# Optimization experiments

Measured on AMD Instinct MI355X. Metric: run time of the kernel, lower is better.

## Reference

```python
import jax, jax.numpy as jnp
import numpy as np

# ---- constants mirroring ATSSPostProcessor defaults / metainfo ----
PRE_NMS_THRESH = 0.05
PRE_NMS_TOP_N = 1000
NMS_THRESH = 0.6
POST_TOP_N = 100
IMG_H, IMG_W = 800.0, 1216.0      # metainfo img_shape
BW_XY, BW_WH = 10.0, 5.0          # GLIP/ATSS box coder weights (10,10,5,5)
MAX_DWH = float(np.log(1000.0 / 16.0))
CLASS_OFFSET = 10000.0            # batched_nms class offset (> max coord)


def setup_inputs() -> dict:
    key = jax.random.key(0)
    k0, k1, k2, k3 = jax.random.split(key, 4)
    N, C, L, H, W = 8, 80, 256, 100, 152
    box_regression = jax.random.normal(k0, (N, 4, H, W), jnp.float32)
    centerness = jax.random.normal(k1, (N, 1, H, W), jnp.float32)
    box_cls = jax.random.normal(k2, (N, C, H, W), jnp.float32)
    dot_product_logits = jax.random.normal(k3, (N, H * W, L), jnp.float32)
    # stride-8 grid anchors with base size 64
    ys, xs = np.meshgrid(np.arange(H), np.arange(W), indexing='ij')
    cx, cy = (xs + 0.5) * 8.0, (ys + 0.5) * 8.0
    anchors = jnp.asarray(
        np.stack([cx - 32, cy - 32, cx + 32, cy + 32], -1).reshape(-1, 4),
        jnp.float32)
    # MEAN aggregation positive map: class j <- tokens [3j, 3j+1, 3j+2]
    pm = np.zeros((C, L), np.float32)
    for j in range(C):
        pm[j, 3 * j:3 * j + 3] = 1.0 / 3.0
    pos_map = jnp.asarray(pm)
    return dict(box_regression=box_regression, centerness=centerness,
                box_cls=box_cls, dot_product_logits=dot_product_logits,
                anchors=anchors, pos_map=pos_map)


def _decode(a, r):
    # delta_xywh decode with weights (10,10,5,5), clamped to img_shape
    aw, ah = a[..., 2] - a[..., 0], a[..., 3] - a[..., 1]
    acx, acy = a[..., 0] + 0.5 * aw, a[..., 1] + 0.5 * ah
    dx, dy = r[..., 0] / BW_XY, r[..., 1] / BW_XY
    dw = jnp.minimum(r[..., 2] / BW_WH, MAX_DWH)
    dh = jnp.minimum(r[..., 3] / BW_WH, MAX_DWH)
    pcx, pcy = dx * aw + acx, dy * ah + acy
    pw, ph = jnp.exp(dw) * aw, jnp.exp(dh) * ah
    x1 = jnp.clip(pcx - 0.5 * pw, 0.0, IMG_W)
    y1 = jnp.clip(pcy - 0.5 * ph, 0.0, IMG_H)
    x2 = jnp.clip(pcx + 0.5 * pw, 0.0, IMG_W)
    y2 = jnp.clip(pcy + 0.5 * ph, 0.0, IMG_H)
    return jnp.stack([x1, y1, x2, y2], -1)


def _iou_matrix(b):  # b: [K,4]
    area = (b[:, 2] - b[:, 0]) * (b[:, 3] - b[:, 1])
    ix1 = jnp.maximum(b[:, None, 0], b[None, :, 0])
    iy1 = jnp.maximum(b[:, None, 1], b[None, :, 1])
    ix2 = jnp.minimum(b[:, None, 2], b[None, :, 2])
    iy2 = jnp.minimum(b[:, None, 3], b[None, :, 3])
    inter = jnp.maximum(ix2 - ix1, 0.0) * jnp.maximum(iy2 - iy1, 0.0)
    return inter / (area[:, None] + area[None, :] - inter + 1e-6)


def _nms_single(boxes, scores, labels, valid):
    # class-aware greedy NMS (batched_nms) on fixed-size K candidates
    K = boxes.shape[0]
    s = jnp.where(valid, scores, -1.0)
    order = jnp.argsort(-s)
    b, s, l, v = boxes[order], s[order], labels[order], valid[order]
    ob = b + (l.astype(b.dtype) * CLASS_OFFSET)[:, None]
    iou = _iou_matrix(ob)
    ar = jnp.arange(K)

    def body(i, keep):
        sup = keep[i] & (iou[i] > NMS_THRESH) & (ar > i)
        return keep & ~sup

    keep = jax.lax.fori_loop(0, K, body, v)
    s2 = jnp.where(keep, s, -1.0)
    topv, topi = jax.lax.top_k(s2, POST_TOP_N)
    good = topv > 0.0
    fb = jnp.where(good[:, None], b[topi], 0.0)
    fs = jnp.where(good, topv, 0.0)
    fl = jnp.where(good, l[topi], 0)
    return fb, fs, fl


def reference(box_regression, centerness, box_cls, dot_product_logits,
              anchors, pos_map):
    N = box_regression.shape[0]
    C = pos_map.shape[0]
    HW = anchors.shape[0]
    # permute_and_flatten: [N,4,H,W] -> [N,HW,4]
    reg = box_regression.transpose(0, 2, 3, 1).reshape(N, HW, 4)
    ctr = jax.nn.sigmoid(centerness.reshape(N, HW))
    # sigmoid score fusion + MEAN grounding->od aggregation
    dp = jax.nn.sigmoid(dot_product_logits)            # [N,HW,L]
    scores = jnp.einsum('nkl,cl->nkc', dp, pos_map)    # [N,HW,C]
    cand = scores > PRE_NMS_THRESH
    fused = scores * ctr[:, :, None]
    # dynamic per-image topk over candidates == fixed-K masked top_k
    masked = jnp.where(cand, fused, -1.0).reshape(N, HW * C)
    vals, idx = jax.lax.top_k(masked, PRE_NMS_TOP_N)   # [N,K]
    valid = jnp.take_along_axis(cand.reshape(N, -1), idx, axis=1)
    loc = idx // C
    labels = idx % C + 1
    a = anchors[loc]                                           # [N,K,4]
    r = jnp.take_along_axis(reg, loc[..., None], axis=1)       # [N,K,4]
    boxes = _decode(a, r)
    sc = jnp.sqrt(jnp.maximum(vals, 0.0))
    w = boxes[..., 2] - boxes[..., 0]
    h = boxes[..., 3] - boxes[..., 1]
    valid = valid & (w > 0) & (h > 0)  # min_size = 0 filter
    # scale_factor = 1.0 -> boxes unchanged
    out_boxes, out_scores, out_labels = jax.vmap(_nms_single)(
        boxes, sc, labels, valid)
    return out_boxes, out_scores, out_labels
```

## Files before the change

kernel.cpp:

```cpp
#include <hip/hip_runtime.h>
#include <hip/hip_bf16.h>

#define NIMG 8
#define NC   80
#define NL   256
#define HWQ  15200
#define TOPK 1000
#define CAP  4096
#define SSORT 2048
#define NPOST 100
#define PERIMG (HWQ * NC)
#define TOTAL (NIMG * PERIMG)
#define NROW 16
#define NBLK (NIMG * HWQ / NROW)
#define PI4  (PERIMG / 4)
#define WPI  (PI4 / 64)
#define NWAVE (NIMG * WPI)
#define CBLK (TOTAL / 4 / 256)

__device__ __forceinline__ unsigned flipKey(float f) {
    unsigned u = __float_as_uint(f);
    return u ^ (((unsigned)((int)u >> 31)) | 0x80000000u);
}
__device__ __forceinline__ float unflipKey(unsigned k) {
    unsigned u = k ^ ((k & 0x80000000u) ? 0x80000000u : 0xFFFFFFFFu);
    return __uint_as_float(u);
}
__device__ __forceinline__ float sigmoidf(float x) {
    return 1.0f / (1.0f + expf(-x));
}

__global__ void kprep(const float* __restrict__ pm, unsigned* nnz,
                      unsigned* tok, float* wt) {
    int c = blockIdx.x * blockDim.x + threadIdx.x;
    if (c >= NC) return;
    int cnt = 0;
    for (int l = 0; l < NL; ++l) {
        float v = pm[c * NL + l];
        if (v != 0.0f) { tok[cnt * NC + c] = l; wt[cnt * NC + c] = v; cnt++; }
    }
    nnz[c] = cnt;
}

__global__ void __launch_bounds__(256)
kscoreh(const float* __restrict__ dp, const float* __restrict__ cent,
        const unsigned* __restrict__ nnz, const unsigned* __restrict__ tok,
        const float* __restrict__ wt, float* __restrict__ scores,
        unsigned* __restrict__ gh) {
    __shared__ unsigned h[4096];
    __shared__ float sctr[NROW];
    int t = threadIdx.x;
    for (int i = t; i < 4096; i += 256) h[i] = 0;
    long long base = (long long)blockIdx.x * NROW;
    if (t < NROW) sctr[t] = sigmoidf(cent[base + t]);
    long long obase = base * NC;
    const float* dpb = dp + base * NL;

    int  rr[5], cc[5], mm[5];
    int  tk[5][3];
    float wv[5][3], xv[5][3];
#pragma unroll
    for (int j = 0; j < 5; ++j) {
        int o = t + j * 256;
        rr[j] = o / NC; cc[j] = o - rr[j] * NC;
        mm[j] = (int)nnz[cc[j]];
    }
#pragma unroll
    for (int j = 0; j < 5; ++j) {
        int c = cc[j];
        tk[j][0] = (int)tok[c]; tk[j][1] = (int)tok[NC + c]; tk[j][2] = (int)tok[2 * NC + c];
        wv[j][0] = wt[c]; wv[j][1] = wt[NC + c]; wv[j][2] = wt[2 * NC + c];
    }
#pragma unroll
    for (int j = 0; j < 5; ++j) {
        const float* row = dpb + rr[j] * NL;
        xv[j][0] = row[tk[j][0]];
        xv[j][1] = row[tk[j][1]];
        xv[j][2] = row[tk[j][2]];
    }
    __syncthreads();
#pragma unroll
    for (int j = 0; j < 5; ++j) {
        float acc = 0.0f;
        if (mm[j] == 3) {
            float s0 = sigmoidf(xv[j][0]);
            float s1 = sigmoidf(xv[j][1]);
            float s2 = sigmoidf(xv[j][2]);
            acc += s0 * wv[j][0]; acc += s1 * wv[j][1]; acc += s2 * wv[j][2];
        } else {
            const float* row = dpb + rr[j] * NL;
            for (int q = 0; q < mm[j]; ++q)
                acc += sigmoidf(row[tok[q * NC + cc[j]]]) * wt[q * NC + cc[j]];
        }
        float sc = (acc > 0.05f) ? acc * sctr[rr[j]] : -1.0f;
        scores[obase + t + j * 256] = sc;
        atomicAdd(&h[flipKey(sc) >> 20], 1u);
    }
    __syncthreads();
    int n = (int)(base / HWQ);
    for (int i = t; i < 4096; i += 256)
        if (h[i]) atomicAdd(&gh[n * 4096 + i], h[i]);
}

__global__ void kfind1(const unsigned* __restrict__ gh, unsigned* meta) {
    __shared__ unsigned h[4096];
    __shared__ unsigned psum[256];
    int n = blockIdx.x;
    for (int i = threadIdx.x; i < 4096; i += 256) h[i] = gh[n * 4096 + i];
    __syncthreads();
    unsigned s = 0;
    for (int i = 0; i < 16; ++i) s += h[threadIdx.x * 16 + i];
    psum[threadIdx.x] = s;
    __syncthreads();
    if (threadIdx.x == 0) {
        unsigned cum = 0, above = 0; int B = 0; bool done = false;
        for (int seg = 255; seg >= 0 && !done; --seg) {
            if (cum + psum[seg] >= TOPK) {
                for (int b = seg * 16 + 15; b >= seg * 16; --b) {
                    if (cum + h[b] >= TOPK) { B = b; above = cum; done = true; break; }
                    cum += h[b];
                }
            } else cum += psum[seg];
        }
        meta[n] = (unsigned)B;
        meta[8 + n] = above;
    }
}

__global__ void __launch_bounds__(256)
kcount(const float4* __restrict__ scores4, const unsigned* __restrict__ meta,
       unsigned* __restrict__ wavecnt) {
    int i4 = blockIdx.x * 256 + threadIdx.x;
    int n = i4 / PI4;
    unsigned B = meta[n];
    float4 v = scores4[i4];
    int ns = 0;
    ns += ((flipKey(v.x) >> 20) >= B);
    ns += ((flipKey(v.y) >> 20) >= B);
    ns += ((flipKey(v.z) >> 20) >= B);
    ns += ((flipKey(v.w) >> 20) >= B);
    int s = ns;
#pragma unroll
    for (int off = 1; off < 64; off <<= 1) s += __shfl_xor(s, off);
    if ((threadIdx.x & 63) == 0) wavecnt[i4 >> 6] = (unsigned)s;
}

__global__ void __launch_bounds__(1024)
kscan(const unsigned* __restrict__ wavecnt, unsigned* __restrict__ waveoff,
      unsigned* __restrict__ cnt) {
    __shared__ unsigned ps[1024];
    int n = blockIdx.x, t = threadIdx.x;
    const unsigned* wc = wavecnt + n * WPI;
    unsigned* wo = waveoff + n * WPI;
    int s0 = t * 5;
    unsigned loc[5]; unsigned sum = 0;
#pragma unroll
    for (int j = 0; j < 5; ++j) {
        int i = s0 + j;
        unsigned vv = (i < WPI) ? wc[i] : 0u;
        loc[j] = sum; sum += vv;
    }
    ps[t] = sum;
    __syncthreads();
    for (int off = 1; off < 1024; off <<= 1) {
        unsigned add = (t >= off) ? ps[t - off] : 0u;
        __syncthreads();
        ps[t] += add;
        __syncthreads();
    }
    unsigned excl = (t > 0) ? ps[t - 1] : 0u;
#pragma unroll
    for (int j = 0; j < 5; ++j) {
        int i = s0 + j;
        if (i < WPI) wo[i] = excl + loc[j];
    }
    if (t == 1023) cnt[n] = ps[1023];
}

__global__ void __launch_bounds__(256)
kwrite(const float4* __restrict__ scores4, const unsigned* __restrict__ meta,
       const unsigned* __restrict__ waveoff, unsigned long long* __restrict__ cand) {
    int i4 = blockIdx.x * 256 + threadIdx.x;
    int n = i4 / PI4;
    unsigned B = meta[n];
    float4 v = scores4[i4];
    int li0 = (i4 - n * PI4) * 4;
    unsigned keys[4]; int sel[4]; int ns = 0;
    keys[0] = flipKey(v.x); sel[0] = (keys[0] >> 20) >= B; ns += sel[0];
    keys[1] = flipKey(v.y); sel[1] = (keys[1] >> 20) >= B; ns += sel[1];
    keys[2] = flipKey(v.z); sel[2] = (keys[2] >> 20) >= B; ns += sel[2];
    keys[3] = flipKey(v.w); sel[3] = (keys[3] >> 20) >= B; ns += sel[3];
    int lane = threadIdx.x & 63;
    int pre = ns;
#pragma unroll
    for (int off = 1; off < 64; off <<= 1) {
        int o = __shfl_up(pre, off);
        if (lane >= off) pre += o;
    }
    unsigned base = waveoff[i4 >> 6] + (unsigned)(pre - ns);
    unsigned long long* cbase = cand + (size_t)n * CAP;
#pragma unroll
    for (int e = 0; e < 4; ++e) {
        if (sel[e]) {
            if (base < CAP)
                cbase[base] = ((unsigned long long)keys[e] << 32)
                              | (unsigned)(~(li0 + e));
            base++;
        }
    }
}

__global__ void __launch_bounds__(1024)
kfine(const unsigned long long* __restrict__ cand, const unsigned* __restrict__ cnt,
      const unsigned* __restrict__ meta, unsigned long long* __restrict__ sorted) {
    __shared__ unsigned h[4096];
    __shared__ unsigned long long sbuf[SSORT];
    __shared__ unsigned psum[256];
    __shared__ unsigned selcnt;
    __shared__ unsigned Fbin;
    int n = blockIdx.x, t = threadIdx.x;
    int M = min(cnt[n], (unsigned)CAP);
    unsigned B = meta[n], above = meta[8 + n];
    const unsigned long long* cb = cand + (size_t)n * CAP;
    for (int i = t; i < 4096; i += 1024) h[i] = 0;
    sbuf[t] = 0ULL; sbuf[t + 1024] = 0ULL;
    if (t == 0) selcnt = 0;
    __syncthreads();
    for (int i = t; i < M; i += 1024) {
        unsigned key = (unsigned)(cb[i] >> 32);
        if ((key >> 20) == B) atomicAdd(&h[(key >> 8) & 0xFFFu], 1u);
    }
    __syncthreads();
    if (t < 256) {
        unsigned s = 0;
        for (int i = 0; i < 16; ++i) s += h[t * 16 + i];
        psum[t] = s;
    }
    __syncthreads();
    if (t == 0) {
        unsigned cum = above; int F = 0; bool done = false;
        for (int seg = 255; seg >= 0 && !done; --seg) {
            if (cum + psum[seg] >= TOPK) {
                for (int b = seg * 16 + 15; b >= seg * 16; --b) {
                    if (cum + h[b] >= TOPK) { F = b; done = true; break; }
                    cum += h[b];
                }
            } else cum += psum[seg];
        }
        Fbin = (unsigned)F;
    }
    __syncthreads();
    unsigned T24 = (B << 12) | Fbin;
    for (int i = t; i < M; i += 1024) {
        unsigned long long e = cb[i];
        unsigned key = (unsigned)(e >> 32);
        if ((key >> 8) >= T24) {
            unsigned p = atomicAdd(&selcnt, 1u);
            if (p < SSORT) sbuf[p] = e;
        }
    }
    __syncthreads();
    int s = (int)selcnt;
    int SN = (s <= 1024) ? 1024 : SSORT;
    for (int k = 2; k <= SN; k <<= 1) {
        for (int j = k >> 1; j > 0; j >>= 1) {
            for (int i = t; i < SN; i += 1024) {
                int l = i ^ j;
                if (l > i) {
                    unsigned long long a = sbuf[i], b = sbuf[l];
                    bool sw = ((i & k) == 0) ? (a < b) : (a > b);
                    if (sw) { sbuf[i] = b; sbuf[l] = a; }
                }
            }
            __syncthreads();
        }
    }
    if (t < TOPK) sorted[(n << 10) + t] = sbuf[t];
}

__global__ void __launch_bounds__(256)
kdecode(const unsigned long long* __restrict__ sorted,
        const float* __restrict__ anchors, const float* __restrict__ breg,
        float4* __restrict__ box4, float4* __restrict__ obx4,
        float* __restrict__ areag, unsigned* __restrict__ lblkeep) {
    int gid = blockIdx.x * 256 + threadIdx.x;
    if (gid >= NIMG * TOPK) return;
    int n = gid / TOPK, r = gid - n * TOPK;
    int o = (n << 10) + r;
    unsigned long long e = sorted[o];
    unsigned key = (unsigned)(e >> 32);
    bool real = key > 0x80000000u;
    unsigned li = ~(unsigned)(e & 0xFFFFFFFFu);
    unsigned k = li / NC, c = li - k * NC;
    int label = (int)c + 1;
    float x1 = 0, y1 = 0, x2 = 0, y2 = 0;
    bool val = false;
    if (real) {
        float a0 = anchors[k * 4 + 0], a1 = anchors[k * 4 + 1];
        float a2 = anchors[k * 4 + 2], a3 = anchors[k * 4 + 3];
        float r0 = breg[(n * 4 + 0) * HWQ + k];
        float r1 = breg[(n * 4 + 1) * HWQ + k];
        float r2 = breg[(n * 4 + 2) * HWQ + k];
        float r3 = breg[(n * 4 + 3) * HWQ + k];
        float aw = a2 - a0, ah = a3 - a1;
        float acx = a0 + 0.5f * aw, acy = a1 + 0.5f * ah;
        float dx = r0 / 10.0f, dy = r1 / 10.0f;
        float dw = fminf(r2 / 5.0f, 4.135166556742356f);
        float dh = fminf(r3 / 5.0f, 4.135166556742356f);
        float pcx = dx * aw + acx, pcy = dy * ah + acy;
        float pw = expf(dw) * aw, ph = expf(dh) * ah;
        x1 = fminf(fmaxf(pcx - 0.5f * pw, 0.0f), 1216.0f);
        y1 = fminf(fmaxf(pcy - 0.5f * ph, 0.0f), 800.0f);
        x2 = fminf(fmaxf(pcx + 0.5f * pw, 0.0f), 1216.0f);
        y2 = fminf(fmaxf(pcy + 0.5f * ph, 0.0f), 800.0f);
        val = (x2 - x1 > 0.0f) && (y2 - y1 > 0.0f);
    }
    box4[o] = make_float4(x1, y1, x2, y2);
    float off = (float)label * 10000.0f;
    float o0 = x1 + off, o1 = y1 + off, o2 = x2 + off, o3 = y2 + off;
    obx4[o] = make_float4(o0, o1, o2, o3);
    areag[o] = (o2 - o0) * (o3 - o1);
    lblkeep[o] = (unsigned)(real ? label : 0) | ((val ? 1u : 0u) << 16);
}

__global__ void __launch_bounds__(1024)
knms2(const unsigned long long* __restrict__ sorted,
      const float4* __restrict__ obx4, const float* __restrict__ areag,
      const unsigned* __restrict__ lblkeep, const float4* __restrict__ box4,
      float* __restrict__ outBoxes, float* __restrict__ outScores,
      float* __restrict__ outLabels) {
    __shared__ float ob0[TOPK], ob1[TOPK], ob2[TOPK], ob3[TOPK], area[TOPK];
    __shared__ unsigned long long sup[TOPK];
    __shared__ unsigned short lbl[TOPK];
    __shared__ unsigned char  keepf[TOPK];
    __shared__ unsigned short wrank[TOPK];
    __shared__ unsigned short clist[TOPK];
    __shared__ unsigned short cstart[NC + 1];
    __shared__ unsigned ccnt[NC];
    __shared__ int pfx[1024];
    __shared__ int smax;

    int n = blockIdx.x, t = threadIdx.x;
    if (t < NC) ccnt[t] = 0;
    if (t == 0) smax = 0;
    if (t < TOPK) {
        int o = (n << 10) + t;
        float4 ob = obx4[o];
        ob0[t] = ob.x; ob1[t] = ob.y; ob2[t] = ob.z; ob3[t] = ob.w;
        area[t] = areag[o];
        unsigned lk = lblkeep[o];
        lbl[t] = (unsigned short)(lk & 0xFFFFu);
        keepf[t] = (unsigned char)(lk >> 16);
        sup[t] = 0ULL;
    }
    __syncthreads();

    if (t < TOPK) {
        unsigned short my = lbl[t];
        int w = 0;
        if (my) {
            for (int r = 0; r < t; ++r) w += (lbl[r] == my);
            atomicAdd(&ccnt[my - 1], 1u);
        }
        wrank[t] = (unsigned short)w;
    }
    __syncthreads();
    if (t < NC) atomicMax(&smax, (int)ccnt[t]);
    __syncthreads();
    if (t == 0) {
        unsigned s = 0;
        for (int c = 0; c < NC; ++c) { cstart[c] = (unsigned short)s; s += ccnt[c]; }
        cstart[NC] = (unsigned short)s;
    }
    __syncthreads();
    if (t < TOPK && lbl[t]) clist[cstart[lbl[t] - 1] + wrank[t]] = (unsigned short)t;
    __syncthreads();

    if (smax <= 64) {
        if (t < TOPK && lbl[t]) {
            int base = cstart[lbl[t] - 1];
            int w = wrank[t];
            float A0 = ob0[t], A1 = ob1[t], A2 = ob2[t], A3 = ob3[t], Aa = area[t];
            unsigned long long m = 0ULL;
            for (int j = 0; j < w; ++j) {
                int ib = clist[base + j];
                float iw = fminf(A2, ob2[ib]) - fmaxf(A0, ob0[ib]);
                float ih = fminf(A3, ob3[ib]) - fmaxf(A1, ob1[ib]);
                float inter = fmaxf(iw, 0.0f) * fmaxf(ih, 0.0f);
                float denom = Aa + area[ib] - inter + 1e-6f;
                if (inter / denom > 0.6f) m |= (1ull << j);
            }
            sup[t] = m;
        }
        __syncthreads();
        if (t < NC) {
            unsigned long long kb = 0ULL;
            int base = cstart[t], mc = (int)ccnt[t];
            for (int w = 0; w < mc; ++w) {
                int i = clist[base + w];
                bool kp = keepf[i] && ((sup[i] & kb) == 0ULL);
                keepf[i] = kp ? 1 : 0;
                if (kp) kb |= (1ull << w);
            }
        }
    } else {
        __syncthreads();
        if (t < NC) {
            int s0 = cstart[t], s1 = s0 + (int)ccnt[t];
            for (int a = s0; a < s1; ++a) {
                int ia = clist[a];
                if (!keepf[ia]) continue;
                float A0 = ob0[ia], A1 = ob1[ia], A2 = ob2[ia], A3 = ob3[ia];
                float Aa = area[ia];
                for (int b = a + 1; b < s1; ++b) {
                    int ib = clist[b];
                    if (!keepf[ib]) continue;
                    float iw = fminf(A2, ob2[ib]) - fmaxf(A0, ob0[ib]);
                    float ih = fminf(A3, ob3[ib]) - fmaxf(A1, ob1[ib]);
                    float inter = fmaxf(iw, 0.0f) * fmaxf(ih, 0.0f);
                    float denom = Aa + area[ib] - inter + 1e-6f;
                    if (inter / denom > 0.6f) keepf[ib] = 0;
                }
            }
        }
    }
    __syncthreads();

    pfx[t] = (t < TOPK) ? (int)keepf[t] : 0;
    __syncthreads();
    for (int off = 1; off < 1024; off <<= 1) {
        int add = (t >= off) ? pfx[t - off] : 0;
        __syncthreads();
        pfx[t] += add;
        __syncthreads();
    }
    int total = pfx[1023];

    if (t < TOPK && keepf[t]) {
        int q = pfx[t] - 1;
        if (q < NPOST) {
            int o = (n << 10) + t;
            float4 b = box4[o];
            float fused = unflipKey((unsigned)(sorted[o] >> 32));
            outBoxes[(n * NPOST + q) * 4 + 0] = b.x;
            outBoxes[(n * NPOST + q) * 4 + 1] = b.y;
            outBoxes[(n * NPOST + q) * 4 + 2] = b.z;
            outBoxes[(n * NPOST + q) * 4 + 3] = b.w;
            outScores[n * NPOST + q] = sqrtf(fmaxf(fused, 0.0f));
            outLabels[n * NPOST + q] = (float)lbl[t];
        }
    }
    if (t < NPOST && t >= total) {
        outBoxes[(n * NPOST + t) * 4 + 0] = 0.0f;
        outBoxes[(n * NPOST + t) * 4 + 1] = 0.0f;
        outBoxes[(n * NPOST + t) * 4 + 2] = 0.0f;
        outBoxes[(n * NPOST + t) * 4 + 3] = 0.0f;
        outScores[n * NPOST + t] = 0.0f;
        outLabels[n * NPOST + t] = 0.0f;
    }
}

extern "C" void kernel_launch(void* const* d_in, const int* in_sizes, int n_in,
                              void* d_out, int out_size, void* d_ws, size_t ws_size,
                              hipStream_t stream) {
    const float* breg = (const float*)d_in[0];
    const float* cent = (const float*)d_in[1];
    const float* dp   = (const float*)d_in[3];
    const float* anc  = (const float*)d_in[4];
    const float* pm   = (const float*)d_in[5];

    char* ws = (char*)d_ws;
    size_t off_scores  = 0;
    size_t off_gh      = off_scores + (size_t)TOTAL * 4;
    size_t off_cnt     = off_gh + (size_t)NIMG * 4096 * 4;
    size_t off_meta    = off_cnt + 128;
    size_t off_cand    = off_meta + 128;
    size_t off_wavecnt = off_cand + (size_t)NIMG * CAP * 8;
    size_t off_waveoff = off_wavecnt + (size_t)NWAVE * 4 + 64;
    size_t off_nnz     = off_waveoff + (size_t)NWAVE * 4 + 64;
    size_t off_tok     = off_nnz + 512;
    size_t off_wt      = off_tok + (size_t)NC * NL * 4;
    size_t needed      = off_wt + (size_t)NC * NL * 4;
    if (ws_size < needed) return;

    size_t off_sorted = off_scores;
    size_t off_box4   = off_sorted + (size_t)NIMG * 1024 * 8;
    size_t off_obx4   = off_box4 + (size_t)NIMG * 1024 * 16;
    size_t off_area   = off_obx4 + (size_t)NIMG * 1024 * 16;
    size_t off_lblk   = off_area + (size_t)NIMG * 1024 * 4;

    float*    scores  = (float*)(ws + off_scores);
    unsigned* gh      = (unsigned*)(ws + off_gh);
    unsigned* cnt     = (unsigned*)(ws + off_cnt);
    unsigned* meta    = (unsigned*)(ws + off_meta);
    unsigned long long* cand = (unsigned long long*)(ws + off_cand);
    unsigned* wavecnt = (unsigned*)(ws + off_wavecnt);
    unsigned* waveoff = (unsigned*)(ws + off_waveoff);
    unsigned* nnz     = (unsigned*)(ws + off_nnz);
    unsigned* tok     = (unsigned*)(ws + off_tok);
    float*    wt      = (float*)(ws + off_wt);
    unsigned long long* sorted = (unsigned long long*)(ws + off_sorted);
    float4*   box4    = (float4*)(ws + off_box4);
    float4*   obx4    = (float4*)(ws + off_obx4);
    float*    areag   = (float*)(ws + off_area);
    unsigned* lblkeep = (unsigned*)(ws + off_lblk);

    hipMemsetAsync(ws + off_gh, 0, (size_t)NIMG * 4096 * 4, stream);

    kprep<<<1, 128, 0, stream>>>(pm, nnz, tok, wt);
    kscoreh<<<NBLK, 256, 0, stream>>>(dp, cent, nnz, tok, wt, scores, gh);
    kfind1<<<NIMG, 256, 0, stream>>>(gh, meta);
    kcount<<<CBLK, 256, 0, stream>>>((const float4*)scores, meta, wavecnt);
    kscan<<<NIMG, 1024, 0, stream>>>(wavecnt, waveoff, cnt);
    kwrite<<<CBLK, 256, 0, stream>>>((const float4*)scores, meta, waveoff, cand);
    kfine<<<NIMG, 1024, 0, stream>>>(cand, cnt, meta, sorted);
    kdecode<<<(NIMG * TOPK + 255) / 256, 256, 0, stream>>>(sorted, anc, breg,
                                                           box4, obx4, areag, lblkeep);

    float* outBoxes  = (float*)d_out;
    float* outScores = outBoxes + NIMG * NPOST * 4;
    float* outLabels = outScores + NIMG * NPOST;
    knms2<<<NIMG, 1024, 0, stream>>>(sorted, obx4, areag, lblkeep, box4,
                                     outBoxes, outScores, outLabels);
}
```

Before: 203.3 us.

## Replace count/scan/write compaction with ballot masks and scan-side scatter

The count pass now stores per-wave ballot masks of selected elements. A new scan kernel walks those masks and writes the candidate keys directly, so the second full pass over the 39 MB scores array (kwrite) is gone. The scoring kernel also moves to 512-thread blocks covering 32 rows and uses a float3 load when a class's three tokens are contiguous. The cost is serial per-thread mask walking and scattered score reads inside only 8 scan blocks, and the new path runs only when the workspace is large enough for the masks.

```diff
diff --git a/kernel.cpp b/kernel.cpp
--- a/kernel.cpp
+++ b/kernel.cpp
@@ -11,8 +11,8 @@
 #define NPOST 100
 #define PERIMG (HWQ * NC)
 #define TOTAL (NIMG * PERIMG)
-#define NROW 16
-#define NBLK (NIMG * HWQ / NROW)
+#define SROW 32
+#define SBLK32 (NIMG * HWQ / SROW)
 #define PI4  (PERIMG / 4)
 #define WPI  (PI4 / 64)
 #define NWAVE (NIMG * WPI)
@@ -42,17 +42,17 @@
     nnz[c] = cnt;
 }
 
-__global__ void __launch_bounds__(256)
+__global__ void __launch_bounds__(512)
 kscoreh(const float* __restrict__ dp, const float* __restrict__ cent,
         const unsigned* __restrict__ nnz, const unsigned* __restrict__ tok,
         const float* __restrict__ wt, float* __restrict__ scores,
         unsigned* __restrict__ gh) {
     __shared__ unsigned h[4096];
-    __shared__ float sctr[NROW];
+    __shared__ float sctr[SROW];
     int t = threadIdx.x;
-    for (int i = t; i < 4096; i += 256) h[i] = 0;
-    long long base = (long long)blockIdx.x * NROW;
-    if (t < NROW) sctr[t] = sigmoidf(cent[base + t]);
+    for (int i = t; i < 4096; i += 512) h[i] = 0;
+    long long base = (long long)blockIdx.x * SROW;
+    if (t < SROW) sctr[t] = sigmoidf(cent[base + t]);
     long long obase = base * NC;
     const float* dpb = dp + base * NL;
 
@@ -61,22 +61,26 @@
     float wv[5][3], xv[5][3];
 #pragma unroll
     for (int j = 0; j < 5; ++j) {
-        int o = t + j * 256;
+        int o = t + j * 512;
         rr[j] = o / NC; cc[j] = o - rr[j] * NC;
         mm[j] = (int)nnz[cc[j]];
-    }
-#pragma unroll
-    for (int j = 0; j < 5; ++j) {
         int c = cc[j];
-        tk[j][0] = (int)tok[c]; tk[j][1] = (int)tok[NC + c]; tk[j][2] = (int)tok[2 * NC + c];
+        tk[j][0] = (int)tok[c] & 255;
+        tk[j][1] = (int)tok[NC + c] & 255;
+        tk[j][2] = (int)tok[2 * NC + c] & 255;
         wv[j][0] = wt[c]; wv[j][1] = wt[NC + c]; wv[j][2] = wt[2 * NC + c];
     }
 #pragma unroll
     for (int j = 0; j < 5; ++j) {
         const float* row = dpb + rr[j] * NL;
-        xv[j][0] = row[tk[j][0]];
-        xv[j][1] = row[tk[j][1]];
-        xv[j][2] = row[tk[j][2]];
+        if (tk[j][1] == tk[j][0] + 1 && tk[j][2] == tk[j][0] + 2) {
+            float3 v3 = *(const float3*)(row + tk[j][0]);
+            xv[j][0] = v3.x; xv[j][1] = v3.y; xv[j][2] = v3.z;
+        } else {
+            xv[j][0] = row[tk[j][0]];
+            xv[j][1] = row[tk[j][1]];
+            xv[j][2] = row[tk[j][2]];
+        }
     }
     __syncthreads();
 #pragma unroll
@@ -93,12 +97,12 @@
                 acc += sigmoidf(row[tok[q * NC + cc[j]]]) * wt[q * NC + cc[j]];
         }
         float sc = (acc > 0.05f) ? acc * sctr[rr[j]] : -1.0f;
-        scores[obase + t + j * 256] = sc;
+        scores[obase + t + j * 512] = sc;
         atomicAdd(&h[flipKey(sc) >> 20], 1u);
     }
     __syncthreads();
     int n = (int)(base / HWQ);
-    for (int i = t; i < 4096; i += 256)
+    for (int i = t; i < 4096; i += 512)
         if (h[i]) atomicAdd(&gh[n * 4096 + i], h[i]);
 }
 
@@ -124,6 +128,83 @@
         }
         meta[n] = (unsigned)B;
         meta[8 + n] = above;
+    }
+}
+
+__global__ void __launch_bounds__(256)
+kcountM(const float4* __restrict__ scores4, const unsigned* __restrict__ meta,
+        unsigned* __restrict__ wavecnt, unsigned long long* __restrict__ wavemask) {
+    int i4 = blockIdx.x * 256 + threadIdx.x;
+    int n = i4 / PI4;
+    unsigned B = meta[n];
+    float4 v = scores4[i4];
+    bool s0 = (flipKey(v.x) >> 20) >= B;
+    bool s1 = (flipKey(v.y) >> 20) >= B;
+    bool s2 = (flipKey(v.z) >> 20) >= B;
+    bool s3 = (flipKey(v.w) >> 20) >= B;
+    unsigned long long m0 = __ballot(s0);
+    unsigned long long m1 = __ballot(s1);
+    unsigned long long m2 = __ballot(s2);
+    unsigned long long m3 = __ballot(s3);
+    if ((threadIdx.x & 63) == 0) {
+        int w = i4 >> 6;
+        wavemask[(size_t)w * 4 + 0] = m0;
+        wavemask[(size_t)w * 4 + 1] = m1;
+        wavemask[(size_t)w * 4 + 2] = m2;
+        wavemask[(size_t)w * 4 + 3] = m3;
+        wavecnt[w] = (unsigned)(__popcll(m0) + __popcll(m1)
+                              + __popcll(m2) + __popcll(m3));
+    }
+}
+
+__global__ void __launch_bounds__(1024)
+kscanW(const unsigned* __restrict__ wavecnt,
+       const unsigned long long* __restrict__ wavemask,
+       const float* __restrict__ scores,
+       unsigned* __restrict__ cnt, unsigned long long* __restrict__ cand) {
+    __shared__ unsigned ps[1024];
+    int n = blockIdx.x, t = threadIdx.x;
+    const unsigned* wc = wavecnt + n * WPI;
+    int s0 = t * 5;
+    unsigned loc[5], vv[5]; unsigned sum = 0;
+#pragma unroll
+    for (int j = 0; j < 5; ++j) {
+        int i = s0 + j;
+        unsigned x = (i < WPI) ? wc[i] : 0u;
+        vv[j] = x; loc[j] = sum; sum += x;
+    }
+    ps[t] = sum;
+    __syncthreads();
+    for (int off = 1; off < 1024; off <<= 1) {
+        unsigned add = (t >= off) ? ps[t - off] : 0u;
+        __syncthreads();
+        ps[t] += add;
+        __syncthreads();
+    }
+    unsigned excl = (t > 0) ? ps[t - 1] : 0u;
+    if (t == 1023) cnt[n] = ps[1023];
+    const float* sb = scores + (size_t)n * PERIMG;
+    unsigned long long* cb = cand + (size_t)n * CAP;
+#pragma unroll
+    for (int j = 0; j < 5; ++j) {
+        int wl = s0 + j;
+        if (wl < WPI && vv[j]) {
+            unsigned off = excl + loc[j];
+            const unsigned long long* mk = wavemask + ((size_t)(n * WPI + wl)) * 4;
+#pragma unroll
+            for (int e = 0; e < 4; ++e) {
+                unsigned long long m = mk[e];
+                while (m) {
+                    int b = __ffsll(m) - 1; m &= m - 1;
+                    int li = wl * 256 + b * 4 + e;
+                    unsigned key = flipKey(sb[li]);
+                    if (off < CAP)
+                        cb[off] = ((unsigned long long)key << 32)
+                                  | (unsigned)(~li);
+                    off++;
+                }
+            }
+        }
     }
 }
 
@@ -144,7 +225,6 @@
     for (int off = 1; off < 64; off <<= 1) s += __shfl_xor(s, off);
     if ((threadIdx.x & 63) == 0) wavecnt[i4 >> 6] = (unsigned)s;
 }
-
 __global__ void __launch_bounds__(1024)
 kscan(const unsigned* __restrict__ wavecnt, unsigned* __restrict__ waveoff,
       unsigned* __restrict__ cnt) {
@@ -176,7 +256,6 @@
     }
     if (t == 1023) cnt[n] = ps[1023];
 }
-
 __global__ void __launch_bounds__(256)
 kwrite(const float4* __restrict__ scores4, const unsigned* __restrict__ meta,
        const unsigned* __restrict__ waveoff, unsigned long long* __restrict__ cand) {
@@ -475,13 +554,15 @@
     size_t off_cnt     = off_gh + (size_t)NIMG * 4096 * 4;
     size_t off_meta    = off_cnt + 128;
     size_t off_cand    = off_meta + 128;
-    size_t off_wavecnt = off_cand + (size_t)NIMG * CAP * 8;
-    size_t off_waveoff = off_wavecnt + (size_t)NWAVE * 4 + 64;
-    size_t off_nnz     = off_waveoff + (size_t)NWAVE * 4 + 64;
+    size_t off_nnz     = off_cand + (size_t)NIMG * CAP * 8;
     size_t off_tok     = off_nnz + 512;
     size_t off_wt      = off_tok + (size_t)NC * NL * 4;
-    size_t needed      = off_wt + (size_t)NC * NL * 4;
-    if (ws_size < needed) return;
+    size_t off_wavecnt = off_wt + (size_t)NC * NL * 4;
+    size_t off_tail    = off_wavecnt + (size_t)NWAVE * 4 + 64;
+    size_t needed_new  = off_tail + (size_t)NWAVE * 32;
+    size_t needed_old  = off_tail + (size_t)NWAVE * 4 + 64;
+    if (ws_size < needed_old) return;
+    bool useMask = ws_size >= needed_new;
 
     size_t off_sorted = off_scores;
     size_t off_box4   = off_sorted + (size_t)NIMG * 1024 * 8;
@@ -494,11 +575,12 @@
     unsigned* cnt     = (unsigned*)(ws + off_cnt);
     unsigned* meta    = (unsigned*)(ws + off_meta);
     unsigned long long* cand = (unsigned long long*)(ws + off_cand);
-    unsigned* wavecnt = (unsigned*)(ws + off_wavecnt);
-    unsigned* waveoff = (unsigned*)(ws + off_waveoff);
     unsigned* nnz     = (unsigned*)(ws + off_nnz);
     unsigned* tok     = (unsigned*)(ws + off_tok);
     float*    wt      = (float*)(ws + off_wt);
+    unsigned* wavecnt = (unsigned*)(ws + off_wavecnt);
+    unsigned long long* wavemask = (unsigned long long*)(ws + off_tail);
+    unsigned* waveoff = (unsigned*)(ws + off_tail);
     unsigned long long* sorted = (unsigned long long*)(ws + off_sorted);
     float4*   box4    = (float4*)(ws + off_box4);
     float4*   obx4    = (float4*)(ws + off_obx4);
@@ -508,11 +590,17 @@
     hipMemsetAsync(ws + off_gh, 0, (size_t)NIMG * 4096 * 4, stream);
 
     kprep<<<1, 128, 0, stream>>>(pm, nnz, tok, wt);
-    kscoreh<<<NBLK, 256, 0, stream>>>(dp, cent, nnz, tok, wt, scores, gh);
+    kscoreh<<<SBLK32, 512, 0, stream>>>(dp, cent, nnz, tok, wt, scores, gh);
     kfind1<<<NIMG, 256, 0, stream>>>(gh, meta);
-    kcount<<<CBLK, 256, 0, stream>>>((const float4*)scores, meta, wavecnt);
-    kscan<<<NIMG, 1024, 0, stream>>>(wavecnt, waveoff, cnt);
-    kwrite<<<CBLK, 256, 0, stream>>>((const float4*)scores, meta, waveoff, cand);
+    if (useMask) {
+        kcountM<<<CBLK, 256, 0, stream>>>((const float4*)scores, meta,
+                                          wavecnt, wavemask);
+        kscanW<<<NIMG, 1024, 0, stream>>>(wavecnt, wavemask, scores, cnt, cand);
+    } else {
+        kcount<<<CBLK, 256, 0, stream>>>((const float4*)scores, meta, wavecnt);
+        kscan<<<NIMG, 1024, 0, stream>>>(wavecnt, waveoff, cnt);
+        kwrite<<<CBLK, 256, 0, stream>>>((const float4*)scores, meta, waveoff, cand);
+    }
     kfine<<<NIMG, 1024, 0, stream>>>(cand, cnt, meta, sorted);
     kdecode<<<(NIMG * TOPK + 255) / 256, 256, 0, stream>>>(sorted, anc, breg,
                                                            box4, obx4, areag, lblkeep);
```

Result: no change. 203.0 us (-0.2%).
